# Optimization experiments

Measured on AMD Instinct MI355X. Metric: run time of the kernel, lower is better.

Reference implementation:

```python
import jax, jax.numpy as jnp
import numpy as np

D_IN = 1024
D_OUT = 1024
NUM_HEADS = 16
HEAD_DIM = D_OUT // NUM_HEADS


def setup_inputs() -> dict:
    key = jax.random.key(0)
    ks = jax.random.split(key, 6)
    s = 0.02
    x = jax.random.normal(ks[0], (2, 2048, D_IN), dtype=jnp.float32)
    Wq = jax.random.normal(ks[1], (D_IN, D_OUT), dtype=jnp.float32) * s
    Wk = jax.random.normal(ks[2], (D_IN, D_OUT), dtype=jnp.float32) * s
    Wv = jax.random.normal(ks[3], (D_IN, D_OUT), dtype=jnp.float32) * s
    Wo = jax.random.normal(ks[4], (D_OUT, D_OUT), dtype=jnp.float32) * s
    bo = jnp.zeros((D_OUT,), dtype=jnp.float32)
    return {"x": x, "Wq": Wq, "Wk": Wk, "Wv": Wv, "Wo": Wo, "bo": bo}


def reference(x, Wq, Wk, Wv, Wo, bo):
    b, n, _ = x.shape
    # project and split heads: [b, h, n, d]
    def heads(W):
        return (x @ W).reshape(b, n, NUM_HEADS, HEAD_DIM).transpose(0, 2, 1, 3)
    q, k, v = heads(Wq), heads(Wk), heads(Wv)
    scores = jnp.einsum("bhqd,bhkd->bhqk", q, k)  # [b,h,n,n]
    causal = jnp.tril(jnp.ones((n, n), dtype=bool))  # True = keep
    scores = jnp.where(causal, scores, -jnp.inf)
    attn = jax.nn.softmax(scores / np.sqrt(HEAD_DIM).astype(np.float32), axis=-1)
    ctx = jnp.einsum("bhqk,bhkd->bhqd", attn, v)
    ctx = ctx.transpose(0, 2, 1, 3).reshape(b, n, D_OUT)
    return ctx @ Wo + bo
```

## Files before the change

kernel.cpp:

```cpp
#include <hip/hip_runtime.h>
#include <stdint.h>

typedef unsigned short u16;
typedef __attribute__((ext_vector_type(8))) __bf16 bf16x8;
typedef __attribute__((ext_vector_type(4))) float f32x4;
typedef __attribute__((ext_vector_type(16))) float f32x16;

#define D_IN 1024
#define NH 16
#define DH 64
#define BATCH 2
#define SEQ 2048

#define QSCL 0.1803368801111244f

#define GLD_LDS16(gp, lp)                                                              \
  __builtin_amdgcn_global_load_lds((__attribute__((address_space(1))) const void*)(gp), \
                                   (__attribute__((address_space(3))) void*)(lp), 16, 0, 0)

__device__ __forceinline__ u16 f2b(float f) {
  union { float ff; uint32_t u; } v; v.ff = f;
  return (u16)((v.u + 0x7fffu + ((v.u >> 16) & 1u)) >> 16);
}

__device__ __forceinline__ float swap32f(float v) { return __shfl_xor(v, 32, 64); }

__device__ __forceinline__ uint32_t cvtpk(float a, float b) {
  uint32_t r;
  asm("v_cvt_pk_bf16_f32 %0, %1, %2" : "=v"(r) : "v"(a), "v"(b));
  return r;
}
__device__ __forceinline__ float fexp2(float x) {
  float r;
  asm("v_exp_f32 %0, %1" : "=v"(r) : "v"(x));
  return r;
}

__global__ __launch_bounds__(256)
void prep_kernel(const float* __restrict__ x, u16* __restrict__ xb,
                 const float* __restrict__ W0, const float* __restrict__ W1,
                 const float* __restrict__ W2, const float* __restrict__ W3,
                 u16* __restrict__ T0, u16* __restrict__ T1,
                 u16* __restrict__ T2, u16* __restrict__ T3) {
  __shared__ float tile[32][33];
  if (blockIdx.x < 4096) {
    const int i = (blockIdx.x * 256 + threadIdx.x) * 4;
    const float4 v = *(const float4*)(x + i);
    uint2 pack;
    pack.x = (uint32_t)f2b(v.x) | ((uint32_t)f2b(v.y) << 16);
    pack.y = (uint32_t)f2b(v.z) | ((uint32_t)f2b(v.w) << 16);
    *(uint2*)(xb + i) = pack;
  } else {
    const int bid2 = blockIdx.x - 4096;
    const float* W; u16* T;
    switch (bid2 >> 10) {
      case 0: W = W0; T = T0; break;
      case 1: W = W1; T = T1; break;
      case 2: W = W2; T = T2; break;
      default: W = W3; T = T3; break;
    }
    const int rem = bid2 & 1023;
    const int n0 = (rem >> 5) * 32, k0 = (rem & 31) * 32;
    const int tx = threadIdx.x & 31, ty = threadIdx.x >> 5;
    #pragma unroll
    for (int i = 0; i < 32; i += 8)
      tile[ty + i][tx] = W[(size_t)(k0 + ty + i) * D_IN + n0 + tx];
    __syncthreads();
    #pragma unroll
    for (int i = 0; i < 32; i += 8)
      T[(size_t)(n0 + ty + i) * D_IN + k0 + tx] = f2b(tile[tx][ty + i]);
  }
}

__device__ __forceinline__ void qkv_compute(
    const u16* __restrict__ AsB, const u16* __restrict__ Bq,
    const u16* __restrict__ Bk, const u16* __restrict__ Bv,
    int wm, int wn, int g, int lm,
    f32x4 accq[4][2], f32x4 acck[4][2], f32x4 accv[4][2]) {
  #pragma unroll
  for (int kk = 0; kk < 2; ++kk) {
    const int slot = ((kk * 4 + g) ^ (lm & 7)) << 3;
    bf16x8 af[4];
    #pragma unroll
    for (int i = 0; i < 4; ++i)
      af[i] = *(const bf16x8*)(AsB + (wm * 64 + i * 16 + lm) * 64 + slot);
    bf16x8 bq[2], bk[2], bv[2];
    #pragma unroll
    for (int n = 0; n < 2; ++n) {
      const int ro = (wn * 32 + n * 16 + lm) * 64 + slot;
      bq[n] = *(const bf16x8*)(Bq + ro);
      bk[n] = *(const bf16x8*)(Bk + ro);
      bv[n] = *(const bf16x8*)(Bv + ro);
    }
    #pragma unroll
    for (int i = 0; i < 4; ++i)
      #pragma unroll
      for (int n = 0; n < 2; ++n) {
        accq[i][n] = __builtin_amdgcn_mfma_f32_16x16x32_bf16(af[i], bq[n], accq[i][n], 0, 0, 0);
        acck[i][n] = __builtin_amdgcn_mfma_f32_16x16x32_bf16(af[i], bk[n], acck[i][n], 0, 0, 0);
        accv[i][n] = __builtin_amdgcn_mfma_f32_16x16x32_bf16(af[i], bv[n], accv[i][n], 0, 0, 0);
      }
  }
}

__global__ __launch_bounds__(512)
void gemm_qkv_kernel(const u16* __restrict__ Xb,
                     const u16* __restrict__ WqT, const u16* __restrict__ WkT,
                     const u16* __restrict__ WvT,
                     u16* __restrict__ Qo, u16* __restrict__ Ko, u16* __restrict__ Vt) {
  __shared__ u16 smem[65536];
  u16* As0 = smem;
  u16* Bs0 = smem + 16384;

  const int tid = threadIdx.x;
  const int lane = tid & 63;
  const int w = tid >> 6;
  const int wm = w >> 2, wn = w & 3;
  const int bm = blockIdx.x * 128;
  const int bn = blockIdx.y * 128;
  const int g = lane >> 4, lm = lane & 15;

  const int r_in = lane >> 3;
  const int s_w = lane & 7;
  const int swz_col = (s_w ^ r_in) << 3;

  const int c0 = w * 2;
  const u16* a_src0 = Xb + (size_t)(bm + c0 * 8 + r_in) * D_IN + swz_col;
  const u16* a_src1 = a_src0 + 8 * D_IN;
  const u16* q_src0 = WqT + (size_t)(bn + c0 * 8 + r_in) * D_IN + swz_col;
  const u16* q_src1 = q_src0 + 8 * D_IN;
  const u16* k_src0 = WkT + (size_t)(bn + c0 * 8 + r_in) * D_IN + swz_col;
  const u16* k_src1 = k_src0 + 8 * D_IN;
  const u16* v_src0 = WvT + (size_t)(bn + c0 * 8 + r_in) * D_IN + swz_col;
  const u16* v_src1 = v_src0 + 8 * D_IN;

#define QKV_STAGE(BUF, K0)                                            \
  do {                                                                \
    GLD_LDS16(a_src0 + (K0), As0 + (BUF)*8192 + c0 * 512);            \
    GLD_LDS16(a_src1 + (K0), As0 + (BUF)*8192 + c0 * 512 + 512);      \
    GLD_LDS16(q_src0 + (K0), Bs0 + (BUF)*24576 + c0 * 512);           \
    GLD_LDS16(q_src1 + (K0), Bs0 + (BUF)*24576 + c0 * 512 + 512);     \
    GLD_LDS16(k_src0 + (K0), Bs0 + (BUF)*24576 + 8192 + c0 * 512);    \
    GLD_LDS16(k_src1 + (K0), Bs0 + (BUF)*24576 + 8192 + c0 * 512 + 512); \
    GLD_LDS16(v_src0 + (K0), Bs0 + (BUF)*24576 + 16384 + c0 * 512);   \
    GLD_LDS16(v_src1 + (K0), Bs0 + (BUF)*24576 + 16384 + c0 * 512 + 512); \
  } while (0)

  f32x4 accq[4][2], acck[4][2], accv[4][2];
  #pragma unroll
  for (int i = 0; i < 4; ++i)
    #pragma unroll
    for (int n = 0; n < 2; ++n) {
      accq[i][n] = {0.f, 0.f, 0.f, 0.f};
      acck[i][n] = {0.f, 0.f, 0.f, 0.f};
      accv[i][n] = {0.f, 0.f, 0.f, 0.f};
    }

  QKV_STAGE(0, 0);
  QKV_STAGE(1, 64);
  #pragma unroll 1
  for (int tt = 0; tt < 7; ++tt) {
    asm volatile("s_waitcnt vmcnt(8)" ::: "memory");
    __builtin_amdgcn_s_barrier();
    qkv_compute(As0, Bs0, Bs0 + 8192, Bs0 + 16384, wm, wn, g, lm, accq, acck, accv);
    __builtin_amdgcn_s_barrier();
    QKV_STAGE(0, (2 * tt + 2) * 64);
    asm volatile("s_waitcnt vmcnt(8)" ::: "memory");
    __builtin_amdgcn_s_barrier();
    qkv_compute(As0 + 8192, Bs0 + 24576, Bs0 + 32768, Bs0 + 40960, wm, wn, g, lm,
                accq, acck, accv);
    __builtin_amdgcn_s_barrier();
    QKV_STAGE(1, (2 * tt + 3) * 64);
  }
  asm volatile("s_waitcnt vmcnt(8)" ::: "memory");
  __builtin_amdgcn_s_barrier();
  qkv_compute(As0, Bs0, Bs0 + 8192, Bs0 + 16384, wm, wn, g, lm, accq, acck, accv);
  asm volatile("s_waitcnt vmcnt(0)" ::: "memory");
  __builtin_amdgcn_s_barrier();
  qkv_compute(As0 + 8192, Bs0 + 24576, Bs0 + 32768, Bs0 + 40960, wm, wn, g, lm,
              accq, acck, accv);
#undef QKV_STAGE

  __syncthreads();
  u16* pool = smem + w * 6144;
  const int M0 = bm + wm * 64;
  const int T0v = (M0 & (SEQ - 1)) >> 5;
  const int C0 = bn + wn * 32;
  const int D0 = C0 & 63;
  const int S0 = D0 >> 4;
  const int d5 = D0 >> 5;
  const int bh = (M0 >> 11) * NH + (C0 >> 6);

  #pragma unroll
  for (int i = 0; i < 4; ++i) {
    const int ti = i >> 1;
    const int nbase = (i & 1) * 16 + g * 4;
    #pragma unroll
    for (int n = 0; n < 2; ++n) {
      #pragma unroll
      for (int r = 0; r < 4; ++r) {
        const int offqk = (ti * 2 + n) * 512 + (((lm >> 3) << 5) + nbase + r) * 8 + (lm & 7);
        pool[offqk] = f2b(accq[i][n][r] * QSCL);
        pool[2048 + offqk] = f2b(acck[i][n][r]);
        const int offv = 4096 + (ti * 2 + (i & 1)) * 512 +
                         ((g & 1) * 32 + n * 16 + lm) * 8 + ((g >> 1) << 2) + r;
        pool[offv] = f2b(accv[i][n][r]);
      }
    }
  }
  asm volatile("s_waitcnt lgkmcnt(0)" ::: "memory");
  #pragma unroll
  for (int fl = 0; fl < 4; ++fl) {
    const int t = T0v + (fl >> 1);
    const int st = S0 + (fl & 1);
    const uint4 vq = *(const uint4*)(pool + fl * 512 + lane * 8);
    *(uint4*)(Qo + ((size_t)(bh * 64 + t) * 4 + st) * 512 + lane * 8) = vq;
    const uint4 vk = *(const uint4*)(pool + 2048 + fl * 512 + lane * 8);
    *(uint4*)(Ko + ((size_t)(bh * 64 + t) * 4 + st) * 512 + lane * 8) = vk;
    const int f = ((fl & 1) << 1) + d5;
    const uint4 vv = *(const uint4*)(pool + 4096 + fl * 512 + lane * 8);
    *(uint4*)(Vt + ((size_t)(bh * 64 + t) * 4 + f) * 512 + lane * 8) = vv;
  }
}

__global__ __launch_bounds__(256)
void attn4_kernel(const u16* __restrict__ Qb, const u16* __restrict__ Kb,
                  const u16* __restrict__ Vt, u16* __restrict__ Ctx) {
  __shared__ float mbuf[4][32][64];
  __shared__ float lbuf[4][32];

  const int tid = threadIdx.x;
  const int lane = tid & 63;
  const int kw = tid >> 6;
  const int ql = lane & 31;
  const int hi = lane >> 5;
  const int bid = blockIdx.x;
  const int c = bid & 7;
  const int r = bid >> 3;
  const int jj = r & 31;
  const int bh = c + 8 * (r >> 5);
  const int b = bh >> 4, h = bh & 15;

  const u16* Qf = Qb + (size_t)bh * 64 * 2048;
  const u16* Kf = Kb + (size_t)bh * 64 * 2048;
  const u16* Vf = Vt + (size_t)bh * 64 * 2048;
  const int lofs = lane * 8;

  #pragma unroll 1
  for (int pass = 0; pass < 2; ++pass) {
    const int qt = pass ? (63 - jj) : jj;
    const int qb0 = qt * 32;

    bf16x8 qf[4];
    {
      const u16* qp = Qf + (size_t)qt * 2048 + lofs;
      #pragma unroll
      for (int st = 0; st < 4; ++st) qf[st] = *(const bf16x8*)(qp + st * 512);
    }

    f32x16 ctx0 = {0,0,0,0,0,0,0,0,0,0,0,0,0,0,0,0};
    f32x16 ctx1 = {0,0,0,0,0,0,0,0,0,0,0,0,0,0,0,0};
    float lacc[4] = {0.f, 0.f, 0.f, 0.f};

    bf16x8 kf[4], vf[4];
    if (kw <= qt) {
      {
        const u16* kp = Kf + (size_t)kw * 2048 + lofs;
        const u16* vp = Vf + (size_t)kw * 2048 + lofs;
        #pragma unroll
        for (int st = 0; st < 4; ++st) kf[st] = *(const bf16x8*)(kp + st * 512);
        #pragma unroll
        for (int f = 0; f < 4; ++f) vf[f] = *(const bf16x8*)(vp + f * 512);
      }
      #pragma unroll 2
      for (int t = kw; t <= qt; t += 4) {
        f32x16 sa = {0,0,0,0,0,0,0,0,0,0,0,0,0,0,0,0};
        f32x16 sb = {0,0,0,0,0,0,0,0,0,0,0,0,0,0,0,0};
        sa = __builtin_amdgcn_mfma_f32_32x32x16_bf16(kf[0], qf[0], sa, 0, 0, 0);
        sb = __builtin_amdgcn_mfma_f32_32x32x16_bf16(kf[2], qf[2], sb, 0, 0, 0);
        sa = __builtin_amdgcn_mfma_f32_32x32x16_bf16(kf[1], qf[1], sa, 0, 0, 0);
        sb = __builtin_amdgcn_mfma_f32_32x32x16_bf16(kf[3], qf[3], sb, 0, 0, 0);

        const int tn = (t + 4 <= qt) ? (t + 4) : qt;
        {
          const u16* kp = Kf + (size_t)tn * 2048 + lofs;
          #pragma unroll
          for (int st = 0; st < 4; ++st) kf[st] = *(const bf16x8*)(kp + st * 512);
        }

        float p[16];
        if (t == qt) {
          #pragma unroll
          for (int cr = 0; cr < 16; ++cr) {
            const int kl = ((cr & 3) + 8 * (cr >> 2)) + 4 * hi;
            p[cr] = (kl > ql) ? 0.f : fexp2(sa[cr] + sb[cr]);
          }
        } else {
          #pragma unroll
          for (int cr = 0; cr < 16; ++cr) p[cr] = fexp2(sa[cr] + sb[cr]);
        }
        #pragma unroll
        for (int cr = 0; cr < 16; ++cr) lacc[cr & 3] += p[cr];

        #pragma unroll
        for (int ks = 0; ks < 2; ++ks) {
          uint4 pw;
          pw.x = cvtpk(p[ks * 8 + 0], p[ks * 8 + 1]);
          pw.y = cvtpk(p[ks * 8 + 2], p[ks * 8 + 3]);
          pw.z = cvtpk(p[ks * 8 + 4], p[ks * 8 + 5]);
          pw.w = cvtpk(p[ks * 8 + 6], p[ks * 8 + 7]);
          union { uint4 u; bf16x8 v; } pa; pa.u = pw;
          ctx0 = __builtin_amdgcn_mfma_f32_32x32x16_bf16(vf[ks * 2 + 0], pa.v, ctx0, 0, 0, 0);
          ctx1 = __builtin_amdgcn_mfma_f32_32x32x16_bf16(vf[ks * 2 + 1], pa.v, ctx1, 0, 0, 0);
        }

        {
          const u16* vp = Vf + (size_t)tn * 2048 + lofs;
          #pragma unroll
          for (int f = 0; f < 4; ++f) vf[f] = *(const bf16x8*)(vp + f * 512);
        }
      }
    }

    const float lloc = (lacc[0] + lacc[1]) + (lacc[2] + lacc[3]);
    const float lwv = lloc + swap32f(lloc);

    #pragma unroll
    for (int grp = 0; grp < 4; ++grp) {
      const int ch = grp * 2 + hi;
      f32x4 t0 = {ctx0[grp * 4 + 0], ctx0[grp * 4 + 1], ctx0[grp * 4 + 2], ctx0[grp * 4 + 3]};
      f32x4 t1 = {ctx1[grp * 4 + 0], ctx1[grp * 4 + 1], ctx1[grp * 4 + 2], ctx1[grp * 4 + 3]};
      *(f32x4*)&mbuf[kw][ql][(ch ^ ql) * 4 & 63]       = t0;
      *(f32x4*)&mbuf[kw][ql][((ch + 8) ^ ql) * 4 & 63] = t1;
    }
    if (lane < 32) lbuf[kw][ql] = lwv;
    __syncthreads();

    {
      const int ch0 = kw * 4 + hi * 2;
      f32x4 a0 = {0.f, 0.f, 0.f, 0.f}, a1 = {0.f, 0.f, 0.f, 0.f};
      #pragma unroll
      for (int p2 = 0; p2 < 4; ++p2) {
        a0 += *(const f32x4*)&mbuf[p2][ql][(ch0 ^ ql) * 4 & 63];
        a1 += *(const f32x4*)&mbuf[p2][ql][((ch0 + 1) ^ ql) * 4 & 63];
      }
      const float lt = (lbuf[0][ql] + lbuf[1][ql]) + (lbuf[2][ql] + lbuf[3][ql]);
      const float inv = __builtin_amdgcn_rcpf(lt);
      uint4 pw;
      pw.x = cvtpk(a0[0] * inv, a0[1] * inv);
      pw.y = cvtpk(a0[2] * inv, a0[3] * inv);
      pw.z = cvtpk(a1[0] * inv, a1[1] * inv);
      pw.w = cvtpk(a1[2] * inv, a1[3] * inv);
      *(uint4*)(Ctx + (size_t)(b * SEQ + qb0 + ql) * 1024 + h * 64 + kw * 16 + hi * 8) = pw;
    }
    __syncthreads();
  }
}

__device__ __forceinline__ void out_compute(
    const u16* __restrict__ AsB, const u16* __restrict__ BsB,
    int wr, int wc, int g, int lm, f32x4 acc[2][4]) {
  #pragma unroll
  for (int kk = 0; kk < 2; ++kk) {
    const int slot = ((kk * 4 + g) ^ (lm & 7)) << 3;
    bf16x8 af[2], bf[4];
    #pragma unroll
    for (int i = 0; i < 2; ++i)
      af[i] = *(const bf16x8*)(AsB + (wr * 32 + i * 16 + lm) * 64 + slot);
    #pragma unroll
    for (int n = 0; n < 4; ++n)
      bf[n] = *(const bf16x8*)(BsB + (wc * 64 + n * 16 + lm) * 64 + slot);
    #pragma unroll
    for (int i = 0; i < 2; ++i)
      #pragma unroll
      for (int n = 0; n < 4; ++n)
        acc[i][n] = __builtin_amdgcn_mfma_f32_16x16x32_bf16(af[i], bf[n], acc[i][n], 0, 0, 0);
  }
}

__global__ __launch_bounds__(256)
void gemm_out_kernel(const u16* __restrict__ Ctx, const u16* __restrict__ WoT,
                     const float* __restrict__ bo, float* __restrict__ out) {
  __shared__ u16 As[2][64 * 64];
  __shared__ u16 Bs[2][128 * 64];
  const int tid = threadIdx.x;
  const int lane = tid & 63;
  const int w = tid >> 6;
  const int bm = blockIdx.x * 64;
  const int bn = blockIdx.y * 128;
  const int wr = w >> 1, wc = w & 1;
  const int g = lane >> 4, lm = lane & 15;

  const int r_in = lane >> 3;
  const int s_w = lane & 7;
  const int swz_col = (s_w ^ r_in) << 3;

  const u16* a_src = Ctx + (size_t)(bm + w * 16 + r_in) * D_IN + swz_col;
  const u16* b_src = WoT + (size_t)(bn + w * 32 + r_in) * D_IN + swz_col;

#define OUT_STAGE(BUF, K0)                                                  \
  do {                                                                      \
    GLD_LDS16(a_src + (K0), &As[BUF][(w * 2) * 512]);                       \
    GLD_LDS16(a_src + 8 * D_IN + (K0), &As[BUF][(w * 2 + 1) * 512]);        \
    _Pragma("unroll")                                                       \
    for (int j = 0; j < 4; ++j)                                             \
      GLD_LDS16(b_src + j * 8 * D_IN + (K0), &Bs[BUF][(w * 4 + j) * 512]);  \
  } while (0)

  f32x4 acc[2][4];
  #pragma unroll
  for (int i = 0; i < 2; ++i)
    #pragma unroll
    for (int n = 0; n < 4; ++n) acc[i][n] = {0.f, 0.f, 0.f, 0.f};

  OUT_STAGE(0, 0);
  OUT_STAGE(1, 64);
  #pragma unroll 1
  for (int tt = 0; tt < 7; ++tt) {
    asm volatile("s_waitcnt vmcnt(6)" ::: "memory");
    __builtin_amdgcn_s_barrier();
    out_compute(As[0], Bs[0], wr, wc, g, lm, acc);
    __builtin_amdgcn_s_barrier();
    OUT_STAGE(0, (2 * tt + 2) * 64);
    asm volatile("s_waitcnt vmcnt(6)" ::: "memory");
    __builtin_amdgcn_s_barrier();
    out_compute(As[1], Bs[1], wr, wc, g, lm, acc);
    __builtin_amdgcn_s_barrier();
    OUT_STAGE(1, (2 * tt + 3) * 64);
  }
  asm volatile("s_waitcnt vmcnt(6)" ::: "memory");
  __builtin_amdgcn_s_barrier();
  out_compute(As[0], Bs[0], wr, wc, g, lm, acc);
  asm volatile("s_waitcnt vmcnt(0)" ::: "memory");
  __builtin_amdgcn_s_barrier();
  out_compute(As[1], Bs[1], wr, wc, g, lm, acc);
#undef OUT_STAGE

  #pragma unroll
  for (int i = 0; i < 2; ++i)
    #pragma unroll
    for (int n = 0; n < 4; ++n)
      #pragma unroll
      for (int r = 0; r < 4; ++r) {
        const int m = bm + wr * 32 + i * 16 + g * 4 + r;
        const int cidx = bn + wc * 64 + n * 16 + lm;
        out[(size_t)m * 1024 + cidx] = acc[i][n][r] + bo[cidx];
      }
}

extern "C" void kernel_launch(void* const* d_in, const int* in_sizes, int n_in,
                              void* d_out, int out_size, void* d_ws, size_t ws_size,
                              hipStream_t stream) {
  (void)in_sizes; (void)n_in; (void)out_size; (void)ws_size;
  const float* x  = (const float*)d_in[0];
  const float* Wq = (const float*)d_in[1];
  const float* Wk = (const float*)d_in[2];
  const float* Wv = (const float*)d_in[3];
  const float* Wo = (const float*)d_in[4];
  const float* bo = (const float*)d_in[5];
  float* out = (float*)d_out;

  char* ws = (char*)d_ws;
  u16* xb  = (u16*)(ws);
  u16* WqT = (u16*)(ws + (8u << 20));
  u16* WkT = (u16*)(ws + (10u << 20));
  u16* WvT = (u16*)(ws + (12u << 20));
  u16* WoT = (u16*)(ws + (14u << 20));
  u16* Qb  = (u16*)(ws + (16u << 20));
  u16* Kb  = (u16*)(ws + (24u << 20));
  u16* Vt  = (u16*)(ws + (32u << 20));
  u16* Ctx = xb;

  prep_kernel<<<dim3(8192), 256, 0, stream>>>(x, xb, Wq, Wk, Wv, Wo, WqT, WkT, WvT, WoT);
  gemm_qkv_kernel<<<dim3(32, 8), 512, 0, stream>>>(xb, WqT, WkT, WvT, Qb, Kb, Vt);
  attn4_kernel<<<dim3(1024), 256, 0, stream>>>(Qb, Kb, Vt, Ctx);
  gemm_out_kernel<<<dim3(64, 8), 256, 0, stream>>>(Ctx, WoT, bo, out);
}
```

Measured before the change: 88.35 us.

## Process paired causal query tiles in one K/V sweep sharing loads

The attention kernel used to handle its two query tiles (jj and 63-jj) in two sequential passes, each streaming K and V from global memory. It now keeps both Q tiles in registers and does a single sweep over key tiles up to the larger tile. Each loaded K/V fragment feeds the short tile while it is still in range, which removes the re-read of K/V for the short tile and the extra pass overhead. The cost is more live registers (two Q sets, four context accumulators), which may lower occupancy, plus a less regular inner loop because of the doA branch.

New measurement: 83.81 us (median of 2 runs). 1.05x faster.

```diff
diff --git a/kernel.cpp b/kernel.cpp
--- a/kernel.cpp
+++ b/kernel.cpp
@@ -224,7 +224,7 @@
 }
 
 __global__ __launch_bounds__(256)
-void attn4_kernel(const u16* __restrict__ Qb, const u16* __restrict__ Kb,
+void attn6_kernel(const u16* __restrict__ Qb, const u16* __restrict__ Kb,
                   const u16* __restrict__ Vt, u16* __restrict__ Ctx) {
   __shared__ float mbuf[4][32][64];
   __shared__ float lbuf[4][32];
@@ -241,95 +241,139 @@
   const int bh = c + 8 * (r >> 5);
   const int b = bh >> 4, h = bh & 15;
 
+  const int qtA = jj;
+  const int qtB = 63 - jj;
+
   const u16* Qf = Qb + (size_t)bh * 64 * 2048;
   const u16* Kf = Kb + (size_t)bh * 64 * 2048;
   const u16* Vf = Vt + (size_t)bh * 64 * 2048;
   const int lofs = lane * 8;
 
+  bf16x8 qfA[4], qfB[4];
+  {
+    const u16* qpA = Qf + (size_t)qtA * 2048 + lofs;
+    const u16* qpB = Qf + (size_t)qtB * 2048 + lofs;
+    #pragma unroll
+    for (int st = 0; st < 4; ++st) {
+      qfA[st] = *(const bf16x8*)(qpA + st * 512);
+      qfB[st] = *(const bf16x8*)(qpB + st * 512);
+    }
+  }
+
+  f32x16 cA0 = {0,0,0,0,0,0,0,0,0,0,0,0,0,0,0,0};
+  f32x16 cA1 = {0,0,0,0,0,0,0,0,0,0,0,0,0,0,0,0};
+  f32x16 cB0 = {0,0,0,0,0,0,0,0,0,0,0,0,0,0,0,0};
+  f32x16 cB1 = {0,0,0,0,0,0,0,0,0,0,0,0,0,0,0,0};
+  float lA[2] = {0.f, 0.f};
+  float lB[2] = {0.f, 0.f};
+
+  bf16x8 kf[4], vf[4];
+  {
+    const u16* kp = Kf + (size_t)kw * 2048 + lofs;
+    const u16* vp = Vf + (size_t)kw * 2048 + lofs;
+    #pragma unroll
+    for (int st = 0; st < 4; ++st) kf[st] = *(const bf16x8*)(kp + st * 512);
+    #pragma unroll
+    for (int f = 0; f < 4; ++f) vf[f] = *(const bf16x8*)(vp + f * 512);
+  }
+
   #pragma unroll 1
-  for (int pass = 0; pass < 2; ++pass) {
-    const int qt = pass ? (63 - jj) : jj;
-    const int qb0 = qt * 32;
-
-    bf16x8 qf[4];
+  for (int t = kw; t <= qtB; t += 4) {
+    const int tn = (t + 4 <= qtB) ? (t + 4) : qtB;
+    const bool doA = (t <= qtA);
+
     {
-      const u16* qp = Qf + (size_t)qt * 2048 + lofs;
-      #pragma unroll
-      for (int st = 0; st < 4; ++st) qf[st] = *(const bf16x8*)(qp + st * 512);
-    }
-
-    f32x16 ctx0 = {0,0,0,0,0,0,0,0,0,0,0,0,0,0,0,0};
-    f32x16 ctx1 = {0,0,0,0,0,0,0,0,0,0,0,0,0,0,0,0};
-    float lacc[4] = {0.f, 0.f, 0.f, 0.f};
-
-    bf16x8 kf[4], vf[4];
-    if (kw <= qt) {
+      f32x16 s = {0,0,0,0,0,0,0,0,0,0,0,0,0,0,0,0};
+      #pragma unroll
+      for (int st = 0; st < 4; ++st)
+        s = __builtin_amdgcn_mfma_f32_32x32x16_bf16(kf[st], qfB[st], s, 0, 0, 0);
+      float p[16];
+      if (t == qtB) {
+        #pragma unroll
+        for (int cr = 0; cr < 16; ++cr) {
+          const int kl = ((cr & 3) + 8 * (cr >> 2)) + 4 * hi;
+          p[cr] = (kl > ql) ? 0.f : fexp2(s[cr]);
+        }
+      } else {
+        #pragma unroll
+        for (int cr = 0; cr < 16; ++cr) p[cr] = fexp2(s[cr]);
+      }
+      #pragma unroll
+      for (int cr = 0; cr < 16; ++cr) lB[cr & 1] += p[cr];
+      #pragma unroll
+      for (int ks = 0; ks < 2; ++ks) {
+        uint4 pw;
+        pw.x = cvtpk(p[ks * 8 + 0], p[ks * 8 + 1]);
+        pw.y = cvtpk(p[ks * 8 + 2], p[ks * 8 + 3]);
+        pw.z = cvtpk(p[ks * 8 + 4], p[ks * 8 + 5]);
+        pw.w = cvtpk(p[ks * 8 + 6], p[ks * 8 + 7]);
+        union { uint4 u; bf16x8 v; } pa; pa.u = pw;
+        cB0 = __builtin_amdgcn_mfma_f32_32x32x16_bf16(vf[ks * 2 + 0], pa.v, cB0, 0, 0, 0);
+        cB1 = __builtin_amdgcn_mfma_f32_32x32x16_bf16(vf[ks * 2 + 1], pa.v, cB1, 0, 0, 0);
+      }
+    }
+
+    if (doA) {
+      f32x16 s = {0,0,0,0,0,0,0,0,0,0,0,0,0,0,0,0};
+      #pragma unroll
+      for (int st = 0; st < 4; ++st)
+        s = __builtin_amdgcn_mfma_f32_32x32x16_bf16(kf[st], qfA[st], s, 0, 0, 0);
       {
-        const u16* kp = Kf + (size_t)kw * 2048 + lofs;
-        const u16* vp = Vf + (size_t)kw * 2048 + lofs;
+        const u16* kp = Kf + (size_t)tn * 2048 + lofs;
         #pragma unroll
         for (int st = 0; st < 4; ++st) kf[st] = *(const bf16x8*)(kp + st * 512);
+      }
+      float p[16];
+      if (t == qtA) {
         #pragma unroll
-        for (int f = 0; f < 4; ++f) vf[f] = *(const bf16x8*)(vp + f * 512);
-      }
-      #pragma unroll 2
-      for (int t = kw; t <= qt; t += 4) {
-        f32x16 sa = {0,0,0,0,0,0,0,0,0,0,0,0,0,0,0,0};
-        f32x16 sb = {0,0,0,0,0,0,0,0,0,0,0,0,0,0,0,0};
-        sa = __builtin_amdgcn_mfma_f32_32x32x16_bf16(kf[0], qf[0], sa, 0, 0, 0);
-        sb = __builtin_amdgcn_mfma_f32_32x32x16_bf16(kf[2], qf[2], sb, 0, 0, 0);
-        sa = __builtin_amdgcn_mfma_f32_32x32x16_bf16(kf[1], qf[1], sa, 0, 0, 0);
-        sb = __builtin_amdgcn_mfma_f32_32x32x16_bf16(kf[3], qf[3], sb, 0, 0, 0);
-
-        const int tn = (t + 4 <= qt) ? (t + 4) : qt;
-        {
-          const u16* kp = Kf + (size_t)tn * 2048 + lofs;
-          #pragma unroll
-          for (int st = 0; st < 4; ++st) kf[st] = *(const bf16x8*)(kp + st * 512);
+        for (int cr = 0; cr < 16; ++cr) {
+          const int kl = ((cr & 3) + 8 * (cr >> 2)) + 4 * hi;
+          p[cr] = (kl > ql) ? 0.f : fexp2(s[cr]);
         }
-
-        float p[16];
-        if (t == qt) {
-          #pragma unroll
-          for (int cr = 0; cr < 16; ++cr) {
-            const int kl = ((cr & 3) + 8 * (cr >> 2)) + 4 * hi;
-            p[cr] = (kl > ql) ? 0.f : fexp2(sa[cr] + sb[cr]);
-          }
-        } else {
-          #pragma unroll
-          for (int cr = 0; cr < 16; ++cr) p[cr] = fexp2(sa[cr] + sb[cr]);
-        }
+      } else {
         #pragma unroll
-        for (int cr = 0; cr < 16; ++cr) lacc[cr & 3] += p[cr];
-
-        #pragma unroll
-        for (int ks = 0; ks < 2; ++ks) {
-          uint4 pw;
-          pw.x = cvtpk(p[ks * 8 + 0], p[ks * 8 + 1]);
-          pw.y = cvtpk(p[ks * 8 + 2], p[ks * 8 + 3]);
-          pw.z = cvtpk(p[ks * 8 + 4], p[ks * 8 + 5]);
-          pw.w = cvtpk(p[ks * 8 + 6], p[ks * 8 + 7]);
-          union { uint4 u; bf16x8 v; } pa; pa.u = pw;
-          ctx0 = __builtin_amdgcn_mfma_f32_32x32x16_bf16(vf[ks * 2 + 0], pa.v, ctx0, 0, 0, 0);
-          ctx1 = __builtin_amdgcn_mfma_f32_32x32x16_bf16(vf[ks * 2 + 1], pa.v, ctx1, 0, 0, 0);
-        }
-
-        {
-          const u16* vp = Vf + (size_t)tn * 2048 + lofs;
-          #pragma unroll
-          for (int f = 0; f < 4; ++f) vf[f] = *(const bf16x8*)(vp + f * 512);
-        }
-      }
-    }
-
-    const float lloc = (lacc[0] + lacc[1]) + (lacc[2] + lacc[3]);
-    const float lwv = lloc + swap32f(lloc);
-
+        for (int cr = 0; cr < 16; ++cr) p[cr] = fexp2(s[cr]);
+      }
+      #pragma unroll
+      for (int cr = 0; cr < 16; ++cr) lA[cr & 1] += p[cr];
+      #pragma unroll
+      for (int ks = 0; ks < 2; ++ks) {
+        uint4 pw;
+        pw.x = cvtpk(p[ks * 8 + 0], p[ks * 8 + 1]);
+        pw.y = cvtpk(p[ks * 8 + 2], p[ks * 8 + 3]);
+        pw.z = cvtpk(p[ks * 8 + 4], p[ks * 8 + 5]);
+        pw.w = cvtpk(p[ks * 8 + 6], p[ks * 8 + 7]);
+        union { uint4 u; bf16x8 v; } pa; pa.u = pw;
+        cA0 = __builtin_amdgcn_mfma_f32_32x32x16_bf16(vf[ks * 2 + 0], pa.v, cA0, 0, 0, 0);
+        cA1 = __builtin_amdgcn_mfma_f32_32x32x16_bf16(vf[ks * 2 + 1], pa.v, cA1, 0, 0, 0);
+      }
+    } else {
+      const u16* kp = Kf + (size_t)tn * 2048 + lofs;
+      #pragma unroll
+      for (int st = 0; st < 4; ++st) kf[st] = *(const bf16x8*)(kp + st * 512);
+    }
+
+    {
+      const u16* vp = Vf + (size_t)tn * 2048 + lofs;
+      #pragma unroll
+      for (int f = 0; f < 4; ++f) vf[f] = *(const bf16x8*)(vp + f * 512);
+    }
+  }
+
+  #pragma unroll
+  for (int round = 0; round < 2; ++round) {
+    const f32x16& x0 = round ? cB0 : cA0;
+    const f32x16& x1 = round ? cB1 : cA1;
+    const float ll = round ? (lB[0] + lB[1]) : (lA[0] + lA[1]);
+    const float lwv = ll + swap32f(ll);
+    const int qt = round ? qtB : qtA;
+
+    if (round) __syncthreads();
     #pragma unroll
     for (int grp = 0; grp < 4; ++grp) {
       const int ch = grp * 2 + hi;
-      f32x4 t0 = {ctx0[grp * 4 + 0], ctx0[grp * 4 + 1], ctx0[grp * 4 + 2], ctx0[grp * 4 + 3]};
-      f32x4 t1 = {ctx1[grp * 4 + 0], ctx1[grp * 4 + 1], ctx1[grp * 4 + 2], ctx1[grp * 4 + 3]};
+      f32x4 t0 = {x0[grp * 4 + 0], x0[grp * 4 + 1], x0[grp * 4 + 2], x0[grp * 4 + 3]};
+      f32x4 t1 = {x1[grp * 4 + 0], x1[grp * 4 + 1], x1[grp * 4 + 2], x1[grp * 4 + 3]};
       *(f32x4*)&mbuf[kw][ql][(ch ^ ql) * 4 & 63]       = t0;
       *(f32x4*)&mbuf[kw][ql][((ch + 8) ^ ql) * 4 & 63] = t1;
     }
@@ -351,9 +395,8 @@
       pw.y = cvtpk(a0[2] * inv, a0[3] * inv);
       pw.z = cvtpk(a1[0] * inv, a1[1] * inv);
       pw.w = cvtpk(a1[2] * inv, a1[3] * inv);
-      *(uint4*)(Ctx + (size_t)(b * SEQ + qb0 + ql) * 1024 + h * 64 + kw * 16 + hi * 8) = pw;
-    }
-    __syncthreads();
+      *(uint4*)(Ctx + (size_t)(b * SEQ + qt * 32 + ql) * 1024 + h * 64 + kw * 16 + hi * 8) = pw;
+    }
   }
 }
 
@@ -473,6 +516,6 @@
 
   prep_kernel<<<dim3(8192), 256, 0, stream>>>(x, xb, Wq, Wk, Wv, Wo, WqT, WkT, WvT, WoT);
   gemm_qkv_kernel<<<dim3(32, 8), 512, 0, stream>>>(xb, WqT, WkT, WvT, Qb, Kb, Vt);
-  attn4_kernel<<<dim3(1024), 256, 0, stream>>>(Qb, Kb, Vt, Ctx);
+  attn6_kernel<<<dim3(1024), 256, 0, stream>>>(Qb, Kb, Vt, Ctx);
   gemm_out_kernel<<<dim3(64, 8), 256, 0, stream>>>(Ctx, WoT, bo, out);
 }
```
